# Kernel tuning notes

Measured on AMD Instinct MI355X. Metric: run time of the kernel, lower is better.

Reference implementation:

```python
import jax, jax.numpy as jnp
import numpy as np

DT = 0.001      # time step (matches dt=0.001 in calculate_state)
GAMMA = 2.0     # velocity damping of the relaxation dynamics
L = 1.0         # rest edge length (Strctr.L)


def _energy(x_flat, buckle, thetas_ss, rest_lengths, k_stiff, k_soft, k_stretch):
    """Total potential energy of the 2D chain (rotation hinges + edge stretch)."""
    pos = x_flat.reshape(-1, 2)                    # (N, 2)
    v = pos[1:] - pos[:-1]                         # (E, 2) edge vectors, E = H+1
    edge_len = jnp.sqrt(jnp.sum(v * v, axis=1))    # (E,)
    v1, v2 = v[:-1], v[1:]                         # (H, 2) consecutive edges per hinge
    cross = v1[:, 0] * v2[:, 1] - v1[:, 1] * v2[:, 0]
    dot = jnp.sum(v1 * v2, axis=1)
    thetas = jnp.arctan2(cross, dot)               # (H,) signed hinge angles
    T = thetas[:, None]                            # (H, 1)
    TH = thetas_ss[:, None]                        # (H, 1)
    stiff_mask = ((buckle == 1) & (T > -TH)) | ((buckle == -1) & (T < TH))  # (H, S)
    k_rot = jnp.where(stiff_mask, k_stiff, k_soft)
    rotation_energy = 0.5 * jnp.sum(k_rot * (T - TH) ** 2)
    stretch_energy = 0.5 * jnp.sum(k_stretch * (edge_len - rest_lengths) ** 2)
    return rotation_energy + stretch_energy


def setup_inputs() -> dict:
    key = jax.random.key(0)
    H, S = 32768, 4
    N = H + 2
    k1, k2, k3 = jax.random.split(key, 3)
    # straight chain along x with tiny transverse noise (realistic init geometry)
    base = jnp.stack([jnp.arange(N, dtype=jnp.float32) * L,
                      jnp.zeros((N,), jnp.float32)], axis=1)
    init_pos = base + 0.01 * jax.random.normal(k1, (N, 2), jnp.float32)
    buckle = (2 * jax.random.randint(k2, (H, S), 0, 2) - 1).astype(jnp.int32)  # +/-1
    thetas_ss = 0.2 * jax.random.uniform(k3, (H,), jnp.float32) - 0.1
    rest_lengths = jnp.full((H + 1,), L, dtype=jnp.float32)
    return dict(init_pos=init_pos, buckle=buckle, thetas_ss=thetas_ss,
                rest_lengths=rest_lengths,
                k_stiff=jnp.float32(10.0), k_soft=jnp.float32(0.1),
                k_stretch=jnp.float32(100.0), n_steps=1000)


def reference(init_pos, buckle, thetas_ss, rest_lengths, k_stiff, k_soft, k_stretch, n_steps):
    n_coords = init_pos.size
    # first two nodes (4 DOFs) clamped, tip_loc=None branch
    fixed = jnp.zeros((n_coords,), bool).at[jnp.arange(4)].set(True)
    fixed_vals = init_pos.reshape(-1)
    force = jax.grad(lambda xf: -_energy(xf, buckle, thetas_ss, rest_lengths,
                                         k_stiff, k_soft, k_stretch))
    x0 = init_pos.reshape(-1)
    v0 = jnp.zeros_like(x0)

    def step(carry, _):
        x, v = carry
        f = jnp.where(fixed, 0.0, force(x))                 # potential force on free DOFs
        v = jnp.where(fixed, 0.0, v + DT * (f - GAMMA * v)) # damped semi-implicit Euler
        x = jnp.where(fixed, fixed_vals, x + DT * v)
        return (x, v), x

    (x_final, v_final), pos_in_t = jax.lax.scan(step, (x0, v0), None, length=n_steps)
    return x_final, pos_in_t
```

## Files before the change

### kernel.cpp

```cpp
#include <hip/hip_runtime.h>

#define DT 0.001f
#define GAMMA 2.0f

#define KSTEPS 60
#define HALOB  120
#define TILE   144
#define REGION 384
#define NW     8
#define WINT   48
#define WHALO  8
#define JEXCH  4
#define NTHREADS 512

typedef float v2f __attribute__((ext_vector_type(2)));

__device__ __forceinline__ void lds_barrier() {
    asm volatile("s_waitcnt lgkmcnt(0)" ::: "memory");
    __builtin_amdgcn_s_barrier();
    asm volatile("" ::: "memory");
}

__device__ __forceinline__ float dpp_shl1(float x) {
    return __int_as_float(__builtin_amdgcn_update_dpp(
        0, __float_as_int(x), 0x130, 0xF, 0xF, true));
}
__device__ __forceinline__ float dpp_shr1(float x) {
    return __int_as_float(__builtin_amdgcn_update_dpp(
        0, __float_as_int(x), 0x138, 0xF, 0xF, true));
}

__global__ __launch_bounds__(NTHREADS) void chunk_kernel(
    const float* __restrict__ xin, const float* __restrict__ vin,
    float* __restrict__ xout, float* __restrict__ vout,
    const int*   __restrict__ buckle,
    const float* __restrict__ thetas_ss,
    const float* __restrict__ rest_len,
    const float* __restrict__ kstiff_p,
    const float* __restrict__ ksoft_p,
    const float* __restrict__ kstretch_p,
    const float* __restrict__ init_pos,
    float* __restrict__ out,
    int N, int H, int n_coords, int t0, int ksteps, int n_steps)
{
    __shared__ float4 xch[2][REGION];

    const int lane = threadIdx.x & 63;
    const int w    = threadIdx.x >> 6;
    const int r    = w * WINT + lane - WHALO;
    const int tile_start = blockIdx.x * TILE;
    const int jg   = tile_start - HALOB + r;
    const bool rvalid = (r >= 0) && (r < REGION);
    const bool nvalid = (jg >= 0) && (jg < N);
    const int  jc   = min(max(jg, 0), N - 1);

    const float kS  = kstiff_p[0];
    const float kw  = ksoft_p[0];
    const float kst = kstretch_p[0];

    const bool edge_ok  = (jg >= 0) && (jg <= N - 2);
    const bool hinge_ok = (jg >= 0) && (jg < H);

    const float rl     = rest_len[min(max(jg, 0), H)];
    const float emask  = edge_ok ? 1.0f : 0.0f;
    const float efix   = edge_ok ? 0.0f : 1.0f;
    const float kst_l  = edge_ok ? kst : 0.0f;
    const float kstrl  = kst * rl;
    const float hfix   = hinge_ok ? 0.0f : 1.0f;
    float tss = 0.0f, npf = 0.0f;
    if (hinge_ok) {
        tss = thetas_ss[jg];
        int4 bk = reinterpret_cast<const int4*>(buckle)[jg];
        npf = (float)((bk.x == 1) + (bk.y == 1) + (bk.z == 1) + (bk.w == 1));
    }
    const float ntss  = -tss;
    const float npf4m = 4.0f - npf;
    const float dKl   = hinge_ok ? (kS - kw) : 0.0f;
    const float kw4l  = hinge_ok ? 4.0f * kw : 0.0f;

    const bool pinned = nvalid && (jg < 2);
    v2f pin = {0.0f, 0.0f};
    if (pinned) { pin.x = init_pos[2 * jg]; pin.y = init_pos[2 * jg + 1]; }

    const bool wave_int = (lane >= WHALO) && (lane < WHALO + WINT);
    const bool writer   = wave_int && (r >= HALOB) && (r < HALOB + TILE) && nvalid;

    v2f p, v;
    if (t0 == 0) {
        float2 P0 = reinterpret_cast<const float2*>(init_pos)[jc];
        p.x = P0.x; p.y = P0.y;
        v.x = 0.0f; v.y = 0.0f;
    } else {
        float2 P0 = reinterpret_cast<const float2*>(xin)[jc];
        float2 V0 = reinterpret_cast<const float2*>(vin)[jc];
        p.x = P0.x; p.y = P0.y;
        v.x = V0.x; v.y = V0.y;
    }

    float2* tptr = reinterpret_cast<float2*>(out + (size_t)(t0 + 1) * (size_t)n_coords) + jc;
    const size_t tstride = (size_t)(n_coords / 2);

    const float C998 = 1.0f - GAMMA * DT;

    for (int s0 = 0; s0 < ksteps; s0 += JEXCH) {
        if (s0 > 0) {
            int buf = (s0 >> 2) & 1;
            if (wave_int && rvalid) xch[buf][r] = make_float4(p.x, p.y, v.x, v.y);
            lds_barrier();
            if (rvalid) {
                float4 f4 = xch[buf][r];
                p.x = f4.x; p.y = f4.y; v.x = f4.z; v.y = f4.w;
            }
        }
        float2 sbuf[JEXCH];
        #pragma unroll
        for (int u = 0; u < JEXCH; ++u) {
            v2f q;  q.x  = dpp_shl1(p.x); q.y  = dpp_shl1(p.y);
            v2f e  = q - p;
            v2f en; en.x = dpp_shl1(e.x); en.y = dpp_shl1(e.y);

            float l2   = fmaf(e.x, e.x, fmaf(e.y, e.y, efix));
            float irt  = __builtin_amdgcn_rsqf(l2) * emask;
            float il2  = irt * irt;
            float se   = fmaf(-kstrl, irt, kst_l);

            float cr = e.x * en.y - e.y * en.x;
            float dd = fmaf(e.x, en.x, fmaf(e.y, en.y, hfix));
            float t  = cr * __builtin_amdgcn_rcpf(dd);
            float t2 = t * t;
            float pp = fmaf(t2, 0.11111111f, -0.14285715f);
            pp = fmaf(t2, pp, 0.2f);
            pp = fmaf(t2, pp, -0.33333334f);
            pp = fmaf(t2, pp, 1.0f);
            float th   = pp * t;
            float thmt = th - tss;
            float ns = (th > ntss ? npf : 0.0f) + (th < tss ? npf4m : 0.0f);
            float K  = fmaf(ns, dKl, kw4l);
            float g  = K * thmt;

            float gm   = dpp_shr1(g);
            float coef = (gm - g) * il2;
            v2f F;
            F.x = fmaf(coef, -e.y, se * e.x);
            F.y = fmaf(coef,  e.x, se * e.y);
            v2f Fp; Fp.x = dpp_shr1(F.x); Fp.y = dpp_shr1(F.y);

            v2f f = F - Fp;
            v = v * C998 + f * DT;
            p = p + v * DT;
            if (tile_start == 0) {
                if (pinned) { v.x = 0.0f; v.y = 0.0f; p = pin; }
            }
            sbuf[u] = make_float2(p.x, p.y);
        }
        if (writer) {
            #pragma unroll
            for (int u = 0; u < JEXCH; ++u) {
                tptr[(size_t)u * tstride] = sbuf[u];
            }
        }
        tptr += (size_t)JEXCH * tstride;
    }

    if (writer) {
        reinterpret_cast<float2*>(xout)[jg] = make_float2(p.x, p.y);
        reinterpret_cast<float2*>(vout)[jg] = make_float2(v.x, v.y);
        if (t0 + ksteps == n_steps) {
            reinterpret_cast<float2*>(out)[jg] = make_float2(p.x, p.y);
        }
    }
}

extern "C" void kernel_launch(void* const* d_in, const int* in_sizes, int n_in,
                              void* d_out, int out_size, void* d_ws, size_t ws_size,
                              hipStream_t stream) {
    const float* init_pos  = (const float*)d_in[0];
    const int*   buckle    = (const int*)d_in[1];
    const float* thetas_ss = (const float*)d_in[2];
    const float* rest_len  = (const float*)d_in[3];
    const float* kstiff    = (const float*)d_in[4];
    const float* ksoft     = (const float*)d_in[5];
    const float* kstretch  = (const float*)d_in[6];

    const int n_coords = in_sizes[0];
    const int N = n_coords / 2;
    const int H = in_sizes[2];
    const int n_steps = out_size / n_coords - 1;

    float* out = (float*)d_out;
    float* wsf = (float*)d_ws;
    float* sAx = wsf;
    float* sAv = wsf + n_coords;
    float* sBx = wsf + 2 * n_coords;
    float* sBv = wsf + 3 * n_coords;

    const int nblocks = (N + TILE - 1) / TILE;
    float* xin = sAx; float* vin = sAv;
    float* xout = sBx; float* vout = sBv;
    for (int t0 = 0; t0 < n_steps; t0 += KSTEPS) {
        int k = n_steps - t0; if (k > KSTEPS) k = KSTEPS;
        chunk_kernel<<<nblocks, NTHREADS, 0, stream>>>(
            xin, vin, xout, vout,
            buckle, thetas_ss, rest_len, kstiff, ksoft, kstretch,
            init_pos, out, N, H, n_coords, t0, k, n_steps);
        float* t1 = xin; xin = xout; xout = t1;
        float* t2 = vin; vin = vout; vout = t2;
    }
}
```

Baseline: 285.9 us.

## Process two chain nodes per thread and double the time-step chunk per launch

Each lane now owns a pair of adjacent nodes, so every DPP neighbour exchange covers two nodes and per-lane work doubles. Trajectory stores widen to float4, and the halo depth in node units doubles, allowing 8 steps between LDS exchanges and 120 steps per launch. The goal is fewer blocks, barriers and kernel launches, and a lower halo-recompute ratio. In exchange it uses more registers per lane and a separate LDS array for velocities, and it assumes an even node count (N/2 pairs).

```diff
diff --git a/kernel.cpp b/kernel.cpp
--- a/kernel.cpp
+++ b/kernel.cpp
@@ -3,14 +3,15 @@
 #define DT 0.001f
 #define GAMMA 2.0f
 
-#define KSTEPS 60
-#define HALOB  120
-#define TILE   144
-#define REGION 384
+#define KSTEPS 120
+#define HALOBP 120
+#define TILEP  144
+#define REGP   384
 #define NW     8
 #define WINT   48
 #define WHALO  8
-#define JEXCH  4
+#define JEXCH  8
+#define SBATCH 4
 #define NTHREADS 512
 
 typedef float v2f __attribute__((ext_vector_type(2)));
@@ -31,8 +32,8 @@
 }
 
 __global__ __launch_bounds__(NTHREADS) void chunk_kernel(
-    const float* __restrict__ xin, const float* __restrict__ vin,
-    float* __restrict__ xout, float* __restrict__ vout,
+    const float4* __restrict__ xin, const float4* __restrict__ vin,
+    float4* __restrict__ xout, float4* __restrict__ vout,
     const int*   __restrict__ buckle,
     const float* __restrict__ thetas_ss,
     const float* __restrict__ rest_len,
@@ -43,130 +44,175 @@
     float* __restrict__ out,
     int N, int H, int n_coords, int t0, int ksteps, int n_steps)
 {
-    __shared__ float4 xch[2][REGION];
+    __shared__ float4 xch[2][REGP];
+    __shared__ float4 vch[2][REGP];
 
     const int lane = threadIdx.x & 63;
     const int w    = threadIdx.x >> 6;
-    const int r    = w * WINT + lane - WHALO;
-    const int tile_start = blockIdx.x * TILE;
-    const int jg   = tile_start - HALOB + r;
-    const bool rvalid = (r >= 0) && (r < REGION);
-    const bool nvalid = (jg >= 0) && (jg < N);
-    const int  jc   = min(max(jg, 0), N - 1);
+    const int rp   = w * WINT + lane - WHALO;
+    const int tsp  = blockIdx.x * TILEP;
+    const int jpa  = tsp - HALOBP + rp;
+    const int jga  = 2 * jpa;
+    const int jgb  = jga + 1;
+    const int NP   = N >> 1;
+    const bool rvalid = (rp >= 0) && (rp < REGP);
+    const int  jcp  = min(max(jpa, 0), NP - 1);
 
     const float kS  = kstiff_p[0];
     const float kw  = ksoft_p[0];
     const float kst = kstretch_p[0];
 
-    const bool edge_ok  = (jg >= 0) && (jg <= N - 2);
-    const bool hinge_ok = (jg >= 0) && (jg < H);
-
-    const float rl     = rest_len[min(max(jg, 0), H)];
-    const float emask  = edge_ok ? 1.0f : 0.0f;
-    const float efix   = edge_ok ? 0.0f : 1.0f;
-    const float kst_l  = edge_ok ? kst : 0.0f;
-    const float kstrl  = kst * rl;
-    const float hfix   = hinge_ok ? 0.0f : 1.0f;
-    float tss = 0.0f, npf = 0.0f;
-    if (hinge_ok) {
-        tss = thetas_ss[jg];
-        int4 bk = reinterpret_cast<const int4*>(buckle)[jg];
-        npf = (float)((bk.x == 1) + (bk.y == 1) + (bk.z == 1) + (bk.w == 1));
-    }
-    const float ntss  = -tss;
-    const float npf4m = 4.0f - npf;
-    const float dKl   = hinge_ok ? (kS - kw) : 0.0f;
-    const float kw4l  = hinge_ok ? 4.0f * kw : 0.0f;
-
-    const bool pinned = nvalid && (jg < 2);
-    v2f pin = {0.0f, 0.0f};
-    if (pinned) { pin.x = init_pos[2 * jg]; pin.y = init_pos[2 * jg + 1]; }
+    const bool eokA = (jga >= 0) && (jga <= N - 2);
+    const bool eokB = (jgb >= 0) && (jgb <= N - 2);
+    const bool hokA = (jga >= 0) && (jga < H);
+    const bool hokB = (jgb >= 0) && (jgb < H);
+
+    const float rlA    = rest_len[min(max(jga, 0), H)];
+    const float rlB    = rest_len[min(max(jgb, 0), H)];
+    const float emaskA = eokA ? 1.0f : 0.0f,  emaskB = eokB ? 1.0f : 0.0f;
+    const float efixA  = eokA ? 0.0f : 1.0f,  efixB  = eokB ? 0.0f : 1.0f;
+    const float kstA   = eokA ? kst : 0.0f,   kstB   = eokB ? kst : 0.0f;
+    const float kstrlA = kst * rlA,           kstrlB = kst * rlB;
+    const float hfixA  = hokA ? 0.0f : 1.0f,  hfixB  = hokB ? 0.0f : 1.0f;
+
+    float tssA = 0.f, npfA = 0.f, tssB = 0.f, npfB = 0.f;
+    if (hokA) {
+        tssA = thetas_ss[jga];
+        int4 bk = reinterpret_cast<const int4*>(buckle)[jga];
+        npfA = (float)((bk.x == 1) + (bk.y == 1) + (bk.z == 1) + (bk.w == 1));
+    }
+    if (hokB) {
+        tssB = thetas_ss[jgb];
+        int4 bk = reinterpret_cast<const int4*>(buckle)[jgb];
+        npfB = (float)((bk.x == 1) + (bk.y == 1) + (bk.z == 1) + (bk.w == 1));
+    }
+    const float ntssA = -tssA, ntssB = -tssB;
+    const float npf4A = 4.0f - npfA, npf4B = 4.0f - npfB;
+    const float dKlA  = hokA ? (kS - kw) : 0.0f, dKlB  = hokB ? (kS - kw) : 0.0f;
+    const float kw4A  = hokA ? 4.0f * kw : 0.0f, kw4B  = hokB ? 4.0f * kw : 0.0f;
+
+    const bool pinned = (jpa == 0);
+    float4 pin4 = make_float4(0.f, 0.f, 0.f, 0.f);
+    if (pinned) pin4 = reinterpret_cast<const float4*>(init_pos)[0];
 
     const bool wave_int = (lane >= WHALO) && (lane < WHALO + WINT);
-    const bool writer   = wave_int && (r >= HALOB) && (r < HALOB + TILE) && nvalid;
-
-    v2f p, v;
+    const bool writer   = wave_int && (rp >= HALOBP) && (rp < HALOBP + TILEP)
+                          && (jpa >= 0) && (jpa < NP);
+
+    v2f pa, pb, va, vb;
     if (t0 == 0) {
-        float2 P0 = reinterpret_cast<const float2*>(init_pos)[jc];
-        p.x = P0.x; p.y = P0.y;
-        v.x = 0.0f; v.y = 0.0f;
+        float4 P0 = reinterpret_cast<const float4*>(init_pos)[jcp];
+        pa.x = P0.x; pa.y = P0.y; pb.x = P0.z; pb.y = P0.w;
+        va.x = va.y = vb.x = vb.y = 0.0f;
     } else {
-        float2 P0 = reinterpret_cast<const float2*>(xin)[jc];
-        float2 V0 = reinterpret_cast<const float2*>(vin)[jc];
-        p.x = P0.x; p.y = P0.y;
-        v.x = V0.x; v.y = V0.y;
-    }
-
-    float2* tptr = reinterpret_cast<float2*>(out + (size_t)(t0 + 1) * (size_t)n_coords) + jc;
-    const size_t tstride = (size_t)(n_coords / 2);
+        float4 P0 = xin[jcp];
+        float4 V0 = vin[jcp];
+        pa.x = P0.x; pa.y = P0.y; pb.x = P0.z; pb.y = P0.w;
+        va.x = V0.x; va.y = V0.y; vb.x = V0.z; vb.y = V0.w;
+    }
+
+    float4* tptr = reinterpret_cast<float4*>(out + (size_t)(t0 + 1) * (size_t)n_coords) + jcp;
+    const size_t ts4 = (size_t)(n_coords / 4);
 
     const float C998 = 1.0f - GAMMA * DT;
 
-    for (int s0 = 0; s0 < ksteps; s0 += JEXCH) {
-        if (s0 > 0) {
-            int buf = (s0 >> 2) & 1;
-            if (wave_int && rvalid) xch[buf][r] = make_float4(p.x, p.y, v.x, v.y);
+    for (int s0 = 0; s0 < ksteps; s0 += SBATCH) {
+        if (s0 > 0 && (s0 & (JEXCH - 1)) == 0) {
+            int buf = (s0 >> 3) & 1;
+            if (wave_int && rvalid) {
+                xch[buf][rp] = make_float4(pa.x, pa.y, pb.x, pb.y);
+                vch[buf][rp] = make_float4(va.x, va.y, vb.x, vb.y);
+            }
             lds_barrier();
             if (rvalid) {
-                float4 f4 = xch[buf][r];
-                p.x = f4.x; p.y = f4.y; v.x = f4.z; v.y = f4.w;
-            }
-        }
-        float2 sbuf[JEXCH];
+                float4 f4 = xch[buf][rp];
+                pa.x = f4.x; pa.y = f4.y; pb.x = f4.z; pb.y = f4.w;
+                float4 g4 = vch[buf][rp];
+                va.x = g4.x; va.y = g4.y; vb.x = g4.z; vb.y = g4.w;
+            }
+        }
+        float4 sbuf[SBATCH];
         #pragma unroll
-        for (int u = 0; u < JEXCH; ++u) {
-            v2f q;  q.x  = dpp_shl1(p.x); q.y  = dpp_shl1(p.y);
-            v2f e  = q - p;
-            v2f en; en.x = dpp_shl1(e.x); en.y = dpp_shl1(e.y);
-
-            float l2   = fmaf(e.x, e.x, fmaf(e.y, e.y, efix));
-            float irt  = __builtin_amdgcn_rsqf(l2) * emask;
-            float il2  = irt * irt;
-            float se   = fmaf(-kstrl, irt, kst_l);
-
-            float cr = e.x * en.y - e.y * en.x;
-            float dd = fmaf(e.x, en.x, fmaf(e.y, en.y, hfix));
-            float t  = cr * __builtin_amdgcn_rcpf(dd);
-            float t2 = t * t;
-            float pp = fmaf(t2, 0.11111111f, -0.14285715f);
-            pp = fmaf(t2, pp, 0.2f);
-            pp = fmaf(t2, pp, -0.33333334f);
-            pp = fmaf(t2, pp, 1.0f);
-            float th   = pp * t;
-            float thmt = th - tss;
-            float ns = (th > ntss ? npf : 0.0f) + (th < tss ? npf4m : 0.0f);
-            float K  = fmaf(ns, dKl, kw4l);
-            float g  = K * thmt;
-
-            float gm   = dpp_shr1(g);
-            float coef = (gm - g) * il2;
-            v2f F;
-            F.x = fmaf(coef, -e.y, se * e.x);
-            F.y = fmaf(coef,  e.x, se * e.y);
-            v2f Fp; Fp.x = dpp_shr1(F.x); Fp.y = dpp_shr1(F.y);
-
-            v2f f = F - Fp;
-            v = v * C998 + f * DT;
-            p = p + v * DT;
-            if (tile_start == 0) {
-                if (pinned) { v.x = 0.0f; v.y = 0.0f; p = pin; }
-            }
-            sbuf[u] = make_float2(p.x, p.y);
+        for (int u = 0; u < SBATCH; ++u) {
+            v2f na; na.x = dpp_shl1(pa.x); na.y = dpp_shl1(pa.y);
+            v2f ea = pb - pa;
+            v2f eb = na - pb;
+            v2f ec; ec.x = dpp_shl1(ea.x); ec.y = dpp_shl1(ea.y);
+
+            float l2a  = fmaf(ea.x, ea.x, fmaf(ea.y, ea.y, efixA));
+            float irta = __builtin_amdgcn_rsqf(l2a) * emaskA;
+            float il2a = irta * irta;
+            float sea  = fmaf(-kstrlA, irta, kstA);
+
+            float l2b  = fmaf(eb.x, eb.x, fmaf(eb.y, eb.y, efixB));
+            float irtb = __builtin_amdgcn_rsqf(l2b) * emaskB;
+            float il2b = irtb * irtb;
+            float seb  = fmaf(-kstrlB, irtb, kstB);
+
+            float cra = ea.x * eb.y - ea.y * eb.x;
+            float dda = fmaf(ea.x, eb.x, fmaf(ea.y, eb.y, hfixA));
+            float ta  = cra * __builtin_amdgcn_rcpf(dda);
+            float t2a = ta * ta;
+            float pA = fmaf(t2a, 0.11111111f, -0.14285715f);
+            pA = fmaf(t2a, pA, 0.2f);
+            pA = fmaf(t2a, pA, -0.33333334f);
+            pA = fmaf(t2a, pA, 1.0f);
+            float thA = pA * ta;
+            float nsA = (thA > ntssA ? npfA : 0.0f) + (thA < tssA ? npf4A : 0.0f);
+            float KA  = fmaf(nsA, dKlA, kw4A);
+            float ga  = KA * (thA - tssA);
+
+            float crb = eb.x * ec.y - eb.y * ec.x;
+            float ddb = fmaf(eb.x, ec.x, fmaf(eb.y, ec.y, hfixB));
+            float tb  = crb * __builtin_amdgcn_rcpf(ddb);
+            float t2b = tb * tb;
+            float pB = fmaf(t2b, 0.11111111f, -0.14285715f);
+            pB = fmaf(t2b, pB, 0.2f);
+            pB = fmaf(t2b, pB, -0.33333334f);
+            pB = fmaf(t2b, pB, 1.0f);
+            float thB = pB * tb;
+            float nsB = (thB > ntssB ? npfB : 0.0f) + (thB < tssB ? npf4B : 0.0f);
+            float KB  = fmaf(nsB, dKlB, kw4B);
+            float gb  = KB * (thB - tssB);
+
+            float gprev = dpp_shr1(gb);
+            float coefa = (gprev - ga) * il2a;
+            float coefb = (ga - gb) * il2b;
+            v2f Fa, Fb;
+            Fa.x = fmaf(coefa, -ea.y, sea * ea.x);
+            Fa.y = fmaf(coefa,  ea.x, sea * ea.y);
+            Fb.x = fmaf(coefb, -eb.y, seb * eb.x);
+            Fb.y = fmaf(coefb,  eb.x, seb * eb.y);
+            v2f Fp; Fp.x = dpp_shr1(Fb.x); Fp.y = dpp_shr1(Fb.y);
+
+            v2f fa = Fa - Fp;
+            v2f fb = Fb - Fa;
+            va = va * C998 + fa * DT;
+            pa = pa + va * DT;
+            vb = vb * C998 + fb * DT;
+            pb = pb + vb * DT;
+            if (tsp == 0) {
+                if (pinned) {
+                    va.x = va.y = vb.x = vb.y = 0.0f;
+                    pa.x = pin4.x; pa.y = pin4.y; pb.x = pin4.z; pb.y = pin4.w;
+                }
+            }
+            sbuf[u] = make_float4(pa.x, pa.y, pb.x, pb.y);
         }
         if (writer) {
             #pragma unroll
-            for (int u = 0; u < JEXCH; ++u) {
-                tptr[(size_t)u * tstride] = sbuf[u];
-            }
-        }
-        tptr += (size_t)JEXCH * tstride;
+            for (int u = 0; u < SBATCH; ++u) {
+                tptr[(size_t)u * ts4] = sbuf[u];
+            }
+        }
+        tptr += (size_t)SBATCH * ts4;
     }
 
     if (writer) {
-        reinterpret_cast<float2*>(xout)[jg] = make_float2(p.x, p.y);
-        reinterpret_cast<float2*>(vout)[jg] = make_float2(v.x, v.y);
+        xout[jpa] = make_float4(pa.x, pa.y, pb.x, pb.y);
+        vout[jpa] = make_float4(va.x, va.y, vb.x, vb.y);
         if (t0 + ksteps == n_steps) {
-            reinterpret_cast<float2*>(out)[jg] = make_float2(p.x, p.y);
+            reinterpret_cast<float4*>(out)[jpa] = make_float4(pa.x, pa.y, pb.x, pb.y);
         }
     }
 }
@@ -186,24 +232,24 @@
     const int N = n_coords / 2;
     const int H = in_sizes[2];
     const int n_steps = out_size / n_coords - 1;
+    const int NP = N / 2;
 
     float* out = (float*)d_out;
-    float* wsf = (float*)d_ws;
-    float* sAx = wsf;
-    float* sAv = wsf + n_coords;
-    float* sBx = wsf + 2 * n_coords;
-    float* sBv = wsf + 3 * n_coords;
-
-    const int nblocks = (N + TILE - 1) / TILE;
-    float* xin = sAx; float* vin = sAv;
-    float* xout = sBx; float* vout = sBv;
+    float4* stAx = (float4*)d_ws;
+    float4* stAv = stAx + NP;
+    float4* stBx = stAv + NP;
+    float4* stBv = stBx + NP;
+
+    const int nblocks = (NP + TILEP - 1) / TILEP;
+    float4* xin = stAx; float4* vin = stAv;
+    float4* xout = stBx; float4* vout = stBv;
     for (int t0 = 0; t0 < n_steps; t0 += KSTEPS) {
         int k = n_steps - t0; if (k > KSTEPS) k = KSTEPS;
         chunk_kernel<<<nblocks, NTHREADS, 0, stream>>>(
             xin, vin, xout, vout,
             buckle, thetas_ss, rest_len, kstiff, ksoft, kstretch,
             init_pos, out, N, H, n_coords, t0, k, n_steps);
-        float* t1 = xin; xin = xout; xout = t1;
-        float* t2 = vin; vin = vout; vout = t2;
-    }
-}
+        float4* t1 = xin; xin = xout; xout = t1;
+        float4* t2 = vin; vin = vout; vout = t2;
+    }
+}
```

New measurement: 393.3 us. 1.38x slower.
